# Performance work log

Hardware: AMD Instinct MI355X
Metric: run time of the kernel (lower is better)

The kernel has to match this reference:

```python
import jax, jax.numpy as jnp
import numpy as np

D = 1024      # model dim (used for theta exponent and 1/sqrt(d) scale)
D_H = 128     # head dim


def make_theta():
    # theta[i] = 10 ** (-2*(i-1)/d), each value repeated twice -> length d_H
    i = np.repeat(np.arange(D_H // 2), 2)
    return jnp.asarray(10.0 ** (-2.0 * (i - 1) / D), dtype=jnp.float32)


def rotation(x, theta):
    # x: [B, T, d_H]; positions are 1..T (source uses arange(1, T+1))
    B, T, dh = x.shape
    idx = jnp.arange(1, T + 1, dtype=x.dtype)[:, None]          # [T, 1]
    ang = idx * theta[None, :]                                   # [T, d_H]
    cos, sin = jnp.cos(ang), jnp.sin(ang)
    # pairwise swap with sign: (x0, x1) -> (x1, -x0)
    x2 = x.reshape(B, T, dh // 2, 2)
    swapped = jnp.stack([x2[..., 1], -x2[..., 0]], axis=-1).reshape(B, T, dh)
    return x * cos + swapped * sin


def setup_inputs() -> dict:
    key = jax.random.key(0)
    kx, kq, kk, kv = jax.random.split(key, 4)
    B, T = 4, 2048
    scale = 1.0 / np.sqrt(D)
    return {
        "x": jax.random.normal(kx, (B, T, D), dtype=jnp.float32),
        "Wq": jax.random.normal(kq, (D_H, D), dtype=jnp.float32) * scale,
        "Wk": jax.random.normal(kk, (D_H, D), dtype=jnp.float32) * scale,
        "Wv": jax.random.normal(kv, (D_H, D), dtype=jnp.float32) * scale,
        "theta": make_theta(),
    }


def reference(x, Wq, Wk, Wv, theta):
    B, T, d = x.shape
    Q = jnp.einsum('btd,hd->bth', x, Wq)
    K = jnp.einsum('btd,hd->bth', x, Wk)
    V = jnp.einsum('btd,hd->bth', x, Wv)
    Q = rotation(Q, theta)
    K = rotation(K, theta)
    # scale uses model dim d (not d_H), as in the source
    scores = jnp.einsum('bqh,bkh->bqk', Q, K) * (d ** -0.5)
    causal = jnp.tril(jnp.ones((T, T), dtype=bool))
    scores = jnp.where(causal, scores, -jnp.inf)
    attn = jax.nn.softmax(scores, axis=-1)
    return jnp.einsum('bqk,bkh->bqh', attn, V)
```

## Files before the change

kernel.cpp:

```cpp
#include <hip/hip_runtime.h>
#include <math.h>

#define T_SEQ 2048
#define D_MODEL 1024
#define DH 128
#define SLOTS 288
#define FRAG_B 262144

typedef __bf16 bfx8 __attribute__((ext_vector_type(8)));
typedef float f32x4 __attribute__((ext_vector_type(4)));

union U16x8 { uint4 u4; unsigned int ui[4]; unsigned short us[8]; __bf16 bf[8]; bfx8 v; };

__device__ inline uint4 cvt8u(float4 a, float4 b) {
    U16x8 u;
    u.bf[0] = (__bf16)a.x; u.bf[1] = (__bf16)a.y; u.bf[2] = (__bf16)a.z; u.bf[3] = (__bf16)a.w;
    u.bf[4] = (__bf16)b.x; u.bf[5] = (__bf16)b.y; u.bf[6] = (__bf16)b.z; u.bf[7] = (__bf16)b.w;
    return u.u4;
}

__device__ inline int slot_base32(int qt) {
    int g = qt >> 3, j = qt & 7;
    return 4 * g * (g + 1) + j * (g + 1);
}

__global__ __launch_bounds__(256) void wcvt_kernel(
    const float* __restrict__ Wq, const float* __restrict__ Wk,
    const float* __restrict__ Wv, __bf16* __restrict__ Wb)
{
    const int i = blockIdx.x * 256 + threadIdx.x;
    const int plane = i >> 14;
    const int off = (i & 16383) * 8;
    const float* src = (plane == 0) ? Wq : (plane == 1) ? Wk : Wv;
    float4 a = *(const float4*)(src + off);
    float4 b = *(const float4*)(src + off + 4);
    *(uint4*)&Wb[(size_t)plane * (DH * D_MODEL) + off] = cvt8u(a, b);
}

__global__ __launch_bounds__(256) void qkv_kernel(
    const float* __restrict__ x, const __bf16* __restrict__ Wb,
    const float* __restrict__ theta,
    __bf16* __restrict__ QF, __bf16* __restrict__ KF, __bf16* __restrict__ VF, int M)
{
    __shared__ __align__(16) unsigned short As[2][64 * 72];
    __shared__ __align__(16) unsigned short Bs[2][128 * 72];

    const int ntile = M / 64;
    const int bx = blockIdx.x;
    const int wsel = bx / ntile;
    const int m0 = (bx - wsel * ntile) * 64;

    const int tid = threadIdx.x;
    const int ln = tid & 63, wv = tid >> 6;
    const int lo = ln & 15, quad = ln >> 4;
    const int hi8 = quad * 8;
    const int wm = (wv & 1) * 32;
    const int wn = (wv >> 1) * 64;

    const int arow = tid >> 2, aseg = (tid & 3) * 16;
    const int brow = tid >> 1, bseg = (tid & 1) * 32;
    const float*  axp = x + (size_t)(m0 + arow) * D_MODEL + aseg;
    const __bf16* bwp = Wb + (size_t)wsel * (DH * D_MODEL) + (size_t)brow * D_MODEL + bseg;

    float4 ar[4];
    uint4  br[4];
    #pragma unroll
    for (int q = 0; q < 4; ++q) ar[q] = *(const float4*)(axp + q * 4);
    #pragma unroll
    for (int q = 0; q < 4; ++q) br[q] = *(const uint4*)(bwp + q * 8);

    *(uint4*)&As[0][arow * 72 + aseg]     = cvt8u(ar[0], ar[1]);
    *(uint4*)&As[0][arow * 72 + aseg + 8] = cvt8u(ar[2], ar[3]);
    #pragma unroll
    for (int q = 0; q < 4; ++q) *(uint4*)&Bs[0][brow * 72 + bseg + q * 8] = br[q];
    __syncthreads();

    f32x4 acc[2][4];
    #pragma unroll
    for (int i = 0; i < 2; ++i)
        #pragma unroll
        for (int j = 0; j < 4; ++j) acc[i][j] = (f32x4)(0.f);

    for (int s = 0; s < 16; ++s) {
        const int cur = s & 1;
        if (s < 15) {
            const int kc = (s + 1) * 64;
            #pragma unroll
            for (int q = 0; q < 4; ++q) ar[q] = *(const float4*)(axp + kc + q * 4);
            #pragma unroll
            for (int q = 0; q < 4; ++q) br[q] = *(const uint4*)(bwp + kc + q * 8);
        }

        bfx8 af[2][2], bfr[4][2];
        #pragma unroll
        for (int i = 0; i < 2; ++i)
            #pragma unroll
            for (int s2 = 0; s2 < 2; ++s2)
                af[i][s2] = *(const bfx8*)&As[cur][(wm + i * 16 + lo) * 72 + s2 * 32 + hi8];
        #pragma unroll
        for (int j = 0; j < 4; ++j)
            #pragma unroll
            for (int s2 = 0; s2 < 2; ++s2)
                bfr[j][s2] = *(const bfx8*)&Bs[cur][(wn + j * 16 + lo) * 72 + s2 * 32 + hi8];
        #pragma unroll
        for (int s2 = 0; s2 < 2; ++s2)
            #pragma unroll
            for (int i = 0; i < 2; ++i)
                #pragma unroll
                for (int j = 0; j < 4; ++j)
                    acc[i][j] = __builtin_amdgcn_mfma_f32_16x16x32_bf16(af[i][s2], bfr[j][s2], acc[i][j], 0, 0, 0);

        if (s < 15) {
            const int nxt = cur ^ 1;
            *(uint4*)&As[nxt][arow * 72 + aseg]     = cvt8u(ar[0], ar[1]);
            *(uint4*)&As[nxt][arow * 72 + aseg + 8] = cvt8u(ar[2], ar[3]);
            #pragma unroll
            for (int q = 0; q < 4; ++q) *(uint4*)&Bs[nxt][brow * 72 + bseg + q * 8] = br[q];
            __syncthreads();
        }
    }

    const int b = m0 >> 11;
    const int mloc0 = m0 & (T_SEQ - 1);

    if (wsel < 2) {
        __syncthreads();
        unsigned short* T = &Bs[0][0];
        #pragma unroll
        for (int j = 0; j < 4; ++j) {
            const int h = wn + j * 16 + lo;
            const float th = theta[h];
            #pragma unroll
            for (int i = 0; i < 2; ++i) {
                #pragma unroll
                for (int r = 0; r < 4; ++r) {
                    const int mloc = wm + i * 16 + quad * 4 + r;
                    float v = acc[i][j][r];
                    float partner = __shfl_xor(v, 1, 64);
                    float ang = (float)(mloc0 + mloc + 1) * th;
                    float rev = ang * 0.15915494309189535f;
                    rev -= floorf(rev);
                    float sn = __builtin_amdgcn_sinf(rev);
                    float cs = __builtin_amdgcn_cosf(rev);
                    float res = (h & 1) ? (v * cs - partner * sn)
                                        : (v * cs + partner * sn);
                    U16x8 u; u.bf[0] = (__bf16)res;
                    T[mloc * 136 + h] = u.us[0];
                }
            }
        }
        __syncthreads();
        const int g = tid >> 6, L = tid & 63;
        const int lo2 = L & 15, q2 = L >> 4;
        __bf16* dst = (wsel == 0 ? QF : KF) + (size_t)b * FRAG_B
                    + (size_t)(((mloc0 >> 4) + g) * 4) * 512 + L * 8;
        #pragma unroll
        for (int c4 = 0; c4 < 4; ++c4)
            *(uint4*)(dst + c4 * 512) = *(const uint4*)&T[(g * 16 + lo2) * 136 + c4 * 32 + q2 * 8];
    } else {
        __syncthreads();
        unsigned short* VT = &As[0][0];
        #pragma unroll
        for (int j = 0; j < 4; ++j) {
            const int h = wn + j * 16 + lo;
            #pragma unroll
            for (int i = 0; i < 2; ++i)
                #pragma unroll
                for (int r = 0; r < 4; ++r) {
                    U16x8 u; u.bf[0] = (__bf16)acc[i][j][r];
                    VT[h * 72 + wm + i * 16 + quad * 4 + r] = u.us[0];
                }
        }
        __syncthreads();
        const int g = tid >> 6, L = tid & 63;
        const int lo2 = L & 15, q2 = L >> 4;
        const int kb = mloc0 >> 5;
        #pragma unroll
        for (int f = 0; f < 4; ++f) {
            const int fid = g * 4 + f;
            const int kt = fid >> 3, j = fid & 7;
            __bf16* dst = VF + (size_t)b * FRAG_B + (size_t)((kb + kt) * 8 + j) * 512 + L * 8;
            *(uint4*)dst = *(const uint4*)&VT[(j * 16 + lo2) * 72 + kt * 32 + q2 * 8];
        }
    }
}

__global__ __launch_bounds__(64) void attn_partial_kernel(
    const __bf16* __restrict__ QF, const __bf16* __restrict__ KF,
    const __bf16* __restrict__ VF,
    __bf16* __restrict__ Opb, float* __restrict__ Ll)
{
    const int qt = blockIdx.x, c = blockIdx.y, b = blockIdx.z;
    const int qbase = qt * 32;
    const int kstart = c << 8;
    if (kstart > qbase) return;
    const int nt = min(8, (qbase + 32 - kstart) >> 5);

    __shared__ __align__(16) unsigned short Pw[2 * 640];

    const int ln = threadIdx.x;
    const int lo = ln & 15, quad = ln >> 4;
    const int hi8 = quad * 8;

    const __bf16* QFb = QF + (size_t)b * FRAG_B;
    const __bf16* KFb = KF + (size_t)b * FRAG_B;
    const __bf16* VFb = VF + (size_t)b * FRAG_B;

    bfx8 qf[2][4];
    #pragma unroll
    for (int iq = 0; iq < 2; ++iq)
        #pragma unroll
        for (int c4 = 0; c4 < 4; ++c4)
            qf[iq][c4] = *(const bfx8*)&QFb[(size_t)((qt * 2 + iq) * 4 + c4) * 512 + ln * 8];

    f32x4 O[2][8];
    #pragma unroll
    for (int iq = 0; iq < 2; ++iq)
        #pragma unroll
        for (int j = 0; j < 8; ++j) O[iq][j] = (f32x4)(0.f);
    float lsum[2][4];
    #pragma unroll
    for (int iq = 0; iq < 2; ++iq)
        #pragma unroll
        for (int r = 0; r < 4; ++r) lsum[iq][r] = 0.f;

    for (int kt = 0; kt < nt; ++kt) {
        const int k0 = kstart + kt * 32;
        const int kt16 = k0 >> 4;
        bfx8 kf[2][4], vf[8];
        #pragma unroll
        for (int jj = 0; jj < 2; ++jj)
            #pragma unroll
            for (int c4 = 0; c4 < 4; ++c4)
                kf[jj][c4] = *(const bfx8*)&KFb[(size_t)((kt16 + jj) * 4 + c4) * 512 + ln * 8];
        #pragma unroll
        for (int j = 0; j < 8; ++j)
            vf[j] = *(const bfx8*)&VFb[(size_t)((k0 >> 5) * 8 + j) * 512 + ln * 8];

        f32x4 s4[2][2];
        #pragma unroll
        for (int iq = 0; iq < 2; ++iq)
            #pragma unroll
            for (int jj = 0; jj < 2; ++jj) s4[iq][jj] = (f32x4)(0.f);
        #pragma unroll
        for (int c4 = 0; c4 < 4; ++c4)
            #pragma unroll
            for (int iq = 0; iq < 2; ++iq)
                #pragma unroll
                for (int jj = 0; jj < 2; ++jj)
                    s4[iq][jj] = __builtin_amdgcn_mfma_f32_16x16x32_bf16(qf[iq][c4], kf[jj][c4], s4[iq][jj], 0, 0, 0);

        const bool needMask = (k0 + 31 > qbase);
        #pragma unroll
        for (int iq = 0; iq < 2; ++iq)
            #pragma unroll
            for (int jj = 0; jj < 2; ++jj)
                #pragma unroll
                for (int r = 0; r < 4; ++r) {
                    const int col = k0 + jj * 16 + lo;
                    const int row = qbase + iq * 16 + quad * 4 + r;
                    float p = __expf(s4[iq][jj][r] * 0.03125f);
                    if (needMask && col > row) p = 0.f;
                    lsum[iq][r] += p;
                    U16x8 u; u.bf[0] = (__bf16)p;
                    Pw[iq * 640 + (quad * 4 + r) * 40 + jj * 16 + lo] = u.us[0];
                }

        bfx8 pf0 = *(const bfx8*)&Pw[lo * 40 + hi8];
        bfx8 pf1 = *(const bfx8*)&Pw[640 + lo * 40 + hi8];
        #pragma unroll
        for (int j = 0; j < 8; ++j) {
            O[0][j] = __builtin_amdgcn_mfma_f32_16x16x32_bf16(pf0, vf[j], O[0][j], 0, 0, 0);
            O[1][j] = __builtin_amdgcn_mfma_f32_16x16x32_bf16(pf1, vf[j], O[1][j], 0, 0, 0);
        }
    }

    #pragma unroll
    for (int off = 1; off < 16; off <<= 1)
        #pragma unroll
        for (int iq = 0; iq < 2; ++iq)
            #pragma unroll
            for (int r = 0; r < 4; ++r) lsum[iq][r] += __shfl_xor(lsum[iq][r], off, 64);

    const size_t sb = (size_t)b * SLOTS + slot_base32(qt) + c;
    #pragma unroll
    for (int iq = 0; iq < 2; ++iq)
        #pragma unroll
        for (int j = 0; j < 8; ++j) {
            U16x8 u;
            u.bf[0] = (__bf16)O[iq][j][0]; u.bf[1] = (__bf16)O[iq][j][1];
            u.bf[2] = (__bf16)O[iq][j][2]; u.bf[3] = (__bf16)O[iq][j][3];
            *(uint2*)&Opb[((sb * 2 + iq) * 8 + j) * 256 + ln * 4] = make_uint2(u.ui[0], u.ui[1]);
        }
    if (lo == 0) {
        #pragma unroll
        for (int iq = 0; iq < 2; ++iq)
            #pragma unroll
            for (int r = 0; r < 4; ++r)
                Ll[sb * 32 + iq * 16 + quad * 4 + r] = lsum[iq][r];
    }
}

__global__ __launch_bounds__(128) void attn_merge_kernel(
    const __bf16* __restrict__ Opb, const float* __restrict__ Ll,
    float* __restrict__ out)
{
    const int qt = blockIdx.x, b = blockIdx.y, j = blockIdx.z;
    const int g = qt >> 3, nc = g + 1;
    const size_t base = (size_t)b * SLOTS + slot_base32(qt);

    __shared__ float Lsh[8][32];
    const int tid = threadIdx.x;
    const int iq = tid >> 6, ln = tid & 63;
    const int lo = ln & 15, quad = ln >> 4;

    for (int idx = tid; idx < nc * 32; idx += 128)
        Lsh[idx >> 5][idx & 31] = Ll[(base + (idx >> 5)) * 32 + (idx & 31)];
    __syncthreads();

    float acc[4] = {0.f, 0.f, 0.f, 0.f};
    for (int cc = 0; cc < nc; ++cc) {
        uint2 d = *(const uint2*)&Opb[(((base + cc) * 2 + iq) * 8 + j) * 256 + ln * 4];
        U16x8 u; u.ui[0] = d.x; u.ui[1] = d.y;
        #pragma unroll
        for (int r = 0; r < 4; ++r) acc[r] += (float)u.bf[r];
    }

    #pragma unroll
    for (int r = 0; r < 4; ++r) {
        const int row = iq * 16 + quad * 4 + r;
        float l = 0.f;
        for (int cc = 0; cc < nc; ++cc) l += Lsh[cc][row];
        out[((size_t)b * T_SEQ + qt * 32 + row) * DH + j * 16 + lo] = acc[r] / l;
    }
}

extern "C" void kernel_launch(void* const* d_in, const int* in_sizes, int n_in,
                              void* d_out, int out_size, void* d_ws, size_t ws_size,
                              hipStream_t stream) {
    const float* x     = (const float*)d_in[0];
    const float* Wq    = (const float*)d_in[1];
    const float* Wk    = (const float*)d_in[2];
    const float* Wv    = (const float*)d_in[3];
    const float* theta = (const float*)d_in[4];
    float* out = (float*)d_out;

    const int M = in_sizes[0] / D_MODEL;
    const int B = M / T_SEQ;

    __bf16* QF  = (__bf16*)d_ws;
    __bf16* KF  = QF + (size_t)B * FRAG_B;
    __bf16* VF  = KF + (size_t)B * FRAG_B;
    __bf16* Opb = VF + (size_t)B * FRAG_B;
    float*  Ll  = (float*)(Opb + (size_t)B * SLOTS * 2 * 8 * 256);
    __bf16* Wb  = Opb;

    wcvt_kernel<<<dim3(192), 256, 0, stream>>>(Wq, Wk, Wv, Wb);
    qkv_kernel<<<dim3(3 * (M / 64)), 256, 0, stream>>>(x, Wb, theta, QF, KF, VF, M);
    attn_partial_kernel<<<dim3(T_SEQ / 32, 8, B), 64, 0, stream>>>(QF, KF, VF, Opb, Ll);
    attn_merge_kernel<<<dim3(T_SEQ / 32, B, 8), 128, 0, stream>>>(Opb, Ll, out);
}
```

Before: 126.6 us.

## Replace split-K partial buffers and merge with atomic fp32 accumulation; prefetch K fragments

Partial attention outputs are no longer written as bf16 slots and reduced by a separate merge kernel. Each block now atomically adds its fp32 O and row sums into a zeroed accumulator, and a simple normalize kernel divides by the sum. This drops the slot indexing and the bf16 rounding of partials, but adds a zeroing kernel and many scalar global atomics. K fragments for the next tile are also loaded one iteration ahead to hide load latency.

```diff
diff --git a/kernel.cpp b/kernel.cpp
--- a/kernel.cpp
+++ b/kernel.cpp
@@ -4,7 +4,6 @@
 #define T_SEQ 2048
 #define D_MODEL 1024
 #define DH 128
-#define SLOTS 288
 #define FRAG_B 262144
 
 typedef __bf16 bfx8 __attribute__((ext_vector_type(8)));
@@ -17,11 +16,6 @@
     u.bf[0] = (__bf16)a.x; u.bf[1] = (__bf16)a.y; u.bf[2] = (__bf16)a.z; u.bf[3] = (__bf16)a.w;
     u.bf[4] = (__bf16)b.x; u.bf[5] = (__bf16)b.y; u.bf[6] = (__bf16)b.z; u.bf[7] = (__bf16)b.w;
     return u.u4;
-}
-
-__device__ inline int slot_base32(int qt) {
-    int g = qt >> 3, j = qt & 7;
-    return 4 * g * (g + 1) + j * (g + 1);
 }
 
 __global__ __launch_bounds__(256) void wcvt_kernel(
@@ -35,6 +29,12 @@
     float4 a = *(const float4*)(src + off);
     float4 b = *(const float4*)(src + off + 4);
     *(uint4*)&Wb[(size_t)plane * (DH * D_MODEL) + off] = cvt8u(a, b);
+}
+
+__global__ __launch_bounds__(256) void zero_kernel(float* __restrict__ p)
+{
+    const size_t i = ((size_t)blockIdx.x * 256 + threadIdx.x) * 4;
+    *(float4*)(p + i) = make_float4(0.f, 0.f, 0.f, 0.f);
 }
 
 __global__ __launch_bounds__(256) void qkv_kernel(
@@ -188,7 +188,7 @@
 __global__ __launch_bounds__(64) void attn_partial_kernel(
     const __bf16* __restrict__ QF, const __bf16* __restrict__ KF,
     const __bf16* __restrict__ VF,
-    __bf16* __restrict__ Opb, float* __restrict__ Ll)
+    float* __restrict__ Oacc, float* __restrict__ Lacc)
 {
     const int qt = blockIdx.x, c = blockIdx.y, b = blockIdx.z;
     const int qbase = qt * 32;
@@ -224,18 +224,27 @@
         #pragma unroll
         for (int r = 0; r < 4; ++r) lsum[iq][r] = 0.f;
 
+    bfx8 kcur[2][4], knxt[2][4];
+    #pragma unroll
+    for (int jj = 0; jj < 2; ++jj)
+        #pragma unroll
+        for (int c4 = 0; c4 < 4; ++c4)
+            kcur[jj][c4] = *(const bfx8*)&KFb[(size_t)(((kstart >> 4) + jj) * 4 + c4) * 512 + ln * 8];
+
     for (int kt = 0; kt < nt; ++kt) {
         const int k0 = kstart + kt * 32;
-        const int kt16 = k0 >> 4;
-        bfx8 kf[2][4], vf[8];
-        #pragma unroll
-        for (int jj = 0; jj < 2; ++jj)
-            #pragma unroll
-            for (int c4 = 0; c4 < 4; ++c4)
-                kf[jj][c4] = *(const bfx8*)&KFb[(size_t)((kt16 + jj) * 4 + c4) * 512 + ln * 8];
+        bfx8 vf[8];
         #pragma unroll
         for (int j = 0; j < 8; ++j)
             vf[j] = *(const bfx8*)&VFb[(size_t)((k0 >> 5) * 8 + j) * 512 + ln * 8];
+        if (kt + 1 < nt) {
+            const int kn16 = (k0 + 32) >> 4;
+            #pragma unroll
+            for (int jj = 0; jj < 2; ++jj)
+                #pragma unroll
+                for (int c4 = 0; c4 < 4; ++c4)
+                    knxt[jj][c4] = *(const bfx8*)&KFb[(size_t)((kn16 + jj) * 4 + c4) * 512 + ln * 8];
+        }
 
         f32x4 s4[2][2];
         #pragma unroll
@@ -248,7 +257,7 @@
             for (int iq = 0; iq < 2; ++iq)
                 #pragma unroll
                 for (int jj = 0; jj < 2; ++jj)
-                    s4[iq][jj] = __builtin_amdgcn_mfma_f32_16x16x32_bf16(qf[iq][c4], kf[jj][c4], s4[iq][jj], 0, 0, 0);
+                    s4[iq][jj] = __builtin_amdgcn_mfma_f32_16x16x32_bf16(qf[iq][c4], kcur[jj][c4], s4[iq][jj], 0, 0, 0);
 
         const bool needMask = (k0 + 31 > qbase);
         #pragma unroll
@@ -273,6 +282,11 @@
             O[0][j] = __builtin_amdgcn_mfma_f32_16x16x32_bf16(pf0, vf[j], O[0][j], 0, 0, 0);
             O[1][j] = __builtin_amdgcn_mfma_f32_16x16x32_bf16(pf1, vf[j], O[1][j], 0, 0, 0);
         }
+
+        #pragma unroll
+        for (int jj = 0; jj < 2; ++jj)
+            #pragma unroll
+            for (int c4 = 0; c4 < 4; ++c4) kcur[jj][c4] = knxt[jj][c4];
     }
 
     #pragma unroll
@@ -282,57 +296,40 @@
             #pragma unroll
             for (int r = 0; r < 4; ++r) lsum[iq][r] += __shfl_xor(lsum[iq][r], off, 64);
 
-    const size_t sb = (size_t)b * SLOTS + slot_base32(qt) + c;
+    float* Ob = Oacc + (size_t)b * T_SEQ * DH;
     #pragma unroll
     for (int iq = 0; iq < 2; ++iq)
         #pragma unroll
         for (int j = 0; j < 8; ++j) {
-            U16x8 u;
-            u.bf[0] = (__bf16)O[iq][j][0]; u.bf[1] = (__bf16)O[iq][j][1];
-            u.bf[2] = (__bf16)O[iq][j][2]; u.bf[3] = (__bf16)O[iq][j][3];
-            *(uint2*)&Opb[((sb * 2 + iq) * 8 + j) * 256 + ln * 4] = make_uint2(u.ui[0], u.ui[1]);
+            const int col = j * 16 + lo;
+            #pragma unroll
+            for (int r = 0; r < 4; ++r) {
+                const int row = qbase + iq * 16 + quad * 4 + r;
+                unsafeAtomicAdd(&Ob[(size_t)row * DH + col], O[iq][j][r]);
+            }
         }
     if (lo == 0) {
         #pragma unroll
         for (int iq = 0; iq < 2; ++iq)
             #pragma unroll
             for (int r = 0; r < 4; ++r)
-                Ll[sb * 32 + iq * 16 + quad * 4 + r] = lsum[iq][r];
+                unsafeAtomicAdd(&Lacc[(size_t)b * T_SEQ + qbase + iq * 16 + quad * 4 + r],
+                                lsum[iq][r]);
     }
 }
 
-__global__ __launch_bounds__(128) void attn_merge_kernel(
-    const __bf16* __restrict__ Opb, const float* __restrict__ Ll,
+__global__ __launch_bounds__(256) void normalize_kernel(
+    const float* __restrict__ Oacc, const float* __restrict__ Lacc,
     float* __restrict__ out)
 {
-    const int qt = blockIdx.x, b = blockIdx.y, j = blockIdx.z;
-    const int g = qt >> 3, nc = g + 1;
-    const size_t base = (size_t)b * SLOTS + slot_base32(qt);
-
-    __shared__ float Lsh[8][32];
-    const int tid = threadIdx.x;
-    const int iq = tid >> 6, ln = tid & 63;
-    const int lo = ln & 15, quad = ln >> 4;
-
-    for (int idx = tid; idx < nc * 32; idx += 128)
-        Lsh[idx >> 5][idx & 31] = Ll[(base + (idx >> 5)) * 32 + (idx & 31)];
-    __syncthreads();
-
-    float acc[4] = {0.f, 0.f, 0.f, 0.f};
-    for (int cc = 0; cc < nc; ++cc) {
-        uint2 d = *(const uint2*)&Opb[(((base + cc) * 2 + iq) * 8 + j) * 256 + ln * 4];
-        U16x8 u; u.ui[0] = d.x; u.ui[1] = d.y;
-        #pragma unroll
-        for (int r = 0; r < 4; ++r) acc[r] += (float)u.bf[r];
-    }
-
-    #pragma unroll
-    for (int r = 0; r < 4; ++r) {
-        const int row = iq * 16 + quad * 4 + r;
-        float l = 0.f;
-        for (int cc = 0; cc < nc; ++cc) l += Lsh[cc][row];
-        out[((size_t)b * T_SEQ + qt * 32 + row) * DH + j * 16 + lo] = acc[r] / l;
-    }
+    const int gid = blockIdx.x * 256 + threadIdx.x;
+    const int row = gid >> 4;
+    const int d0  = (gid & 15) * 8;
+    const float inv = 1.f / Lacc[row];
+    float4 a = *(const float4*)(Oacc + (size_t)row * DH + d0);
+    float4 b = *(const float4*)(Oacc + (size_t)row * DH + d0 + 4);
+    *(float4*)(out + (size_t)row * DH + d0)     = make_float4(a.x*inv, a.y*inv, a.z*inv, a.w*inv);
+    *(float4*)(out + (size_t)row * DH + d0 + 4) = make_float4(b.x*inv, b.y*inv, b.z*inv, b.w*inv);
 }
 
 extern "C" void kernel_launch(void* const* d_in, const int* in_sizes, int n_in,
@@ -348,15 +345,16 @@
     const int M = in_sizes[0] / D_MODEL;
     const int B = M / T_SEQ;
 
-    __bf16* QF  = (__bf16*)d_ws;
-    __bf16* KF  = QF + (size_t)B * FRAG_B;
-    __bf16* VF  = KF + (size_t)B * FRAG_B;
-    __bf16* Opb = VF + (size_t)B * FRAG_B;
-    float*  Ll  = (float*)(Opb + (size_t)B * SLOTS * 2 * 8 * 256);
-    __bf16* Wb  = Opb;
+    __bf16* QF   = (__bf16*)d_ws;
+    __bf16* KF   = QF + (size_t)B * FRAG_B;
+    __bf16* VF   = KF + (size_t)B * FRAG_B;
+    float*  Oacc = (float*)(VF + (size_t)B * FRAG_B);
+    float*  Lacc = Oacc + (size_t)B * T_SEQ * DH;
+    __bf16* Wb   = (__bf16*)Oacc;
 
     wcvt_kernel<<<dim3(192), 256, 0, stream>>>(Wq, Wk, Wv, Wb);
     qkv_kernel<<<dim3(3 * (M / 64)), 256, 0, stream>>>(x, Wb, theta, QF, KF, VF, M);
-    attn_partial_kernel<<<dim3(T_SEQ / 32, 8, B), 64, 0, stream>>>(QF, KF, VF, Opb, Ll);
-    attn_merge_kernel<<<dim3(T_SEQ / 32, B, 8), 128, 0, stream>>>(Opb, Ll, out);
-}
+    zero_kernel<<<dim3((B * T_SEQ * DH + B * T_SEQ) / 1024), 256, 0, stream>>>(Oacc);
+    attn_partial_kernel<<<dim3(T_SEQ / 32, 8, B), 64, 0, stream>>>(QF, KF, VF, Oacc, Lacc);
+    normalize_kernel<<<dim3(B * T_SEQ * DH / 2048), 256, 0, stream>>>(Oacc, Lacc, out);
+}
```

After: 133.4 us. +5.4%, slower.

## Pre-convert x and weights to MFMA fragment layout; single-wave QKV GEMM; prefetch K

Applied to the files above, without the earlier changes.

A new prep kernel converts x and the three weight matrices to bf16 and stores them directly in MFMA fragment order. The QKV projection then becomes a 64-thread kernel that streams fragments from global memory with register double buffering and uses no shared-memory staging or block barriers. The attention kernel now prefetches the next K tile into registers while the current one is being processed. The cost is an extra full pass that writes and re-reads x in bf16, plus higher register pressure and a grid of more, smaller blocks.

```diff
diff --git a/kernel.cpp b/kernel.cpp
--- a/kernel.cpp
+++ b/kernel.cpp
@@ -24,99 +24,100 @@
     return 4 * g * (g + 1) + j * (g + 1);
 }
 
-__global__ __launch_bounds__(256) void wcvt_kernel(
+__global__ __launch_bounds__(256) void prep_kernel(
+    const float* __restrict__ x,
     const float* __restrict__ Wq, const float* __restrict__ Wk,
-    const float* __restrict__ Wv, __bf16* __restrict__ Wb)
+    const float* __restrict__ Wv,
+    __bf16* __restrict__ xF, __bf16* __restrict__ WF, int nxb)
 {
-    const int i = blockIdx.x * 256 + threadIdx.x;
-    const int plane = i >> 14;
-    const int off = (i & 16383) * 8;
-    const float* src = (plane == 0) ? Wq : (plane == 1) ? Wk : Wv;
-    float4 a = *(const float4*)(src + off);
-    float4 b = *(const float4*)(src + off + 4);
-    *(uint4*)&Wb[(size_t)plane * (DH * D_MODEL) + off] = cvt8u(a, b);
-}
-
-__global__ __launch_bounds__(256) void qkv_kernel(
-    const float* __restrict__ x, const __bf16* __restrict__ Wb,
+    const int bi = blockIdx.x;
+    const int tid = threadIdx.x;
+
+    if (bi < nxb) {
+        __shared__ __align__(16) unsigned short Xs[64 * 72];
+        const int m0 = (bi >> 4) * 64;
+        const int k0 = (bi & 15) * 64;
+        const int row = tid >> 2, cs = (tid & 3) * 16;
+        const float* xp = x + (size_t)(m0 + row) * D_MODEL + k0 + cs;
+        float4 a0 = *(const float4*)xp;
+        float4 a1 = *(const float4*)(xp + 4);
+        float4 a2 = *(const float4*)(xp + 8);
+        float4 a3 = *(const float4*)(xp + 12);
+        *(uint4*)&Xs[row * 72 + cs]     = cvt8u(a0, a1);
+        *(uint4*)&Xs[row * 72 + cs + 8] = cvt8u(a2, a3);
+        __syncthreads();
+        const int L = tid & 63;
+        #pragma unroll
+        for (int rr = 0; rr < 2; ++rr) {
+            const int fid = rr * 4 + (tid >> 6);
+            const int mtl = fid >> 1, kcl = fid & 1;
+            uint4 d = *(const uint4*)&Xs[(mtl * 16 + (L & 15)) * 72 + kcl * 32 + (L >> 4) * 8];
+            const size_t frag = (size_t)((m0 >> 4) + mtl) * 32 + (k0 >> 5) + kcl;
+            *(uint4*)&xF[frag * 512 + L * 8] = d;
+        }
+    } else {
+        const int i = (bi - nxb) * 256 + tid;
+        const int wsel = i >> 14;
+        const int i2 = i & 16383;
+        const int kc = i2 >> 9, j = (i2 >> 6) & 7, ln = i2 & 63;
+        const int lo = ln & 15, quad = ln >> 4;
+        const float* src = (wsel == 0) ? Wq : (wsel == 1) ? Wk : Wv;
+        const float* p = src + (size_t)(j * 16 + lo) * D_MODEL + kc * 32 + quad * 8;
+        float4 a = *(const float4*)p;
+        float4 b = *(const float4*)(p + 4);
+        *(uint4*)&WF[(size_t)((wsel * 32 + kc) * 8 + j) * 512 + ln * 8] = cvt8u(a, b);
+    }
+}
+
+__global__ __launch_bounds__(64) void qkv_kernel(
+    const __bf16* __restrict__ xF, const __bf16* __restrict__ WF,
     const float* __restrict__ theta,
-    __bf16* __restrict__ QF, __bf16* __restrict__ KF, __bf16* __restrict__ VF, int M)
+    __bf16* __restrict__ QF, __bf16* __restrict__ KF, __bf16* __restrict__ VF)
 {
-    __shared__ __align__(16) unsigned short As[2][64 * 72];
-    __shared__ __align__(16) unsigned short Bs[2][128 * 72];
-
-    const int ntile = M / 64;
+    __shared__ __align__(16) unsigned short T[32 * 136];
+
     const int bx = blockIdx.x;
-    const int wsel = bx / ntile;
-    const int m0 = (bx - wsel * ntile) * 64;
-
-    const int tid = threadIdx.x;
-    const int ln = tid & 63, wv = tid >> 6;
+    const int wsel = bx >> 8;
+    const int m0 = (bx & 255) * 32;
+
+    const int ln = threadIdx.x;
     const int lo = ln & 15, quad = ln >> 4;
-    const int hi8 = quad * 8;
-    const int wm = (wv & 1) * 32;
-    const int wn = (wv >> 1) * 64;
-
-    const int arow = tid >> 2, aseg = (tid & 3) * 16;
-    const int brow = tid >> 1, bseg = (tid & 1) * 32;
-    const float*  axp = x + (size_t)(m0 + arow) * D_MODEL + aseg;
-    const __bf16* bwp = Wb + (size_t)wsel * (DH * D_MODEL) + (size_t)brow * D_MODEL + bseg;
-
-    float4 ar[4];
-    uint4  br[4];
-    #pragma unroll
-    for (int q = 0; q < 4; ++q) ar[q] = *(const float4*)(axp + q * 4);
-    #pragma unroll
-    for (int q = 0; q < 4; ++q) br[q] = *(const uint4*)(bwp + q * 8);
-
-    *(uint4*)&As[0][arow * 72 + aseg]     = cvt8u(ar[0], ar[1]);
-    *(uint4*)&As[0][arow * 72 + aseg + 8] = cvt8u(ar[2], ar[3]);
-    #pragma unroll
-    for (int q = 0; q < 4; ++q) *(uint4*)&Bs[0][brow * 72 + bseg + q * 8] = br[q];
-    __syncthreads();
-
-    f32x4 acc[2][4];
-    #pragma unroll
-    for (int i = 0; i < 2; ++i)
-        #pragma unroll
-        for (int j = 0; j < 4; ++j) acc[i][j] = (f32x4)(0.f);
-
-    for (int s = 0; s < 16; ++s) {
-        const int cur = s & 1;
-        if (s < 15) {
-            const int kc = (s + 1) * 64;
-            #pragma unroll
-            for (int q = 0; q < 4; ++q) ar[q] = *(const float4*)(axp + kc + q * 4);
-            #pragma unroll
-            for (int q = 0; q < 4; ++q) br[q] = *(const uint4*)(bwp + kc + q * 8);
-        }
-
-        bfx8 af[2][2], bfr[4][2];
-        #pragma unroll
-        for (int i = 0; i < 2; ++i)
-            #pragma unroll
-            for (int s2 = 0; s2 < 2; ++s2)
-                af[i][s2] = *(const bfx8*)&As[cur][(wm + i * 16 + lo) * 72 + s2 * 32 + hi8];
-        #pragma unroll
-        for (int j = 0; j < 4; ++j)
-            #pragma unroll
-            for (int s2 = 0; s2 < 2; ++s2)
-                bfr[j][s2] = *(const bfx8*)&Bs[cur][(wn + j * 16 + lo) * 72 + s2 * 32 + hi8];
-        #pragma unroll
-        for (int s2 = 0; s2 < 2; ++s2)
-            #pragma unroll
-            for (int i = 0; i < 2; ++i)
-                #pragma unroll
-                for (int j = 0; j < 4; ++j)
-                    acc[i][j] = __builtin_amdgcn_mfma_f32_16x16x32_bf16(af[i][s2], bfr[j][s2], acc[i][j], 0, 0, 0);
-
-        if (s < 15) {
-            const int nxt = cur ^ 1;
-            *(uint4*)&As[nxt][arow * 72 + aseg]     = cvt8u(ar[0], ar[1]);
-            *(uint4*)&As[nxt][arow * 72 + aseg + 8] = cvt8u(ar[2], ar[3]);
-            #pragma unroll
-            for (int q = 0; q < 4; ++q) *(uint4*)&Bs[nxt][brow * 72 + bseg + q * 8] = br[q];
-            __syncthreads();
+
+    const __bf16* WFp = WF + (size_t)wsel * (32 * 8 * 512);
+    const size_t xf0 = ((size_t)(m0 >> 4)) * 32;
+
+    bfx8 xc[2], xn[2], wc[8], wn[8];
+    #pragma unroll
+    for (int iq = 0; iq < 2; ++iq)
+        xc[iq] = *(const bfx8*)&xF[(xf0 + iq * 32) * 512 + ln * 8];
+    #pragma unroll
+    for (int j = 0; j < 8; ++j)
+        wc[j] = *(const bfx8*)&WFp[(size_t)j * 512 + ln * 8];
+
+    f32x4 acc[2][8];
+    #pragma unroll
+    for (int iq = 0; iq < 2; ++iq)
+        #pragma unroll
+        for (int j = 0; j < 8; ++j) acc[iq][j] = (f32x4)(0.f);
+
+    for (int kc = 0; kc < 32; ++kc) {
+        if (kc < 31) {
+            #pragma unroll
+            for (int iq = 0; iq < 2; ++iq)
+                xn[iq] = *(const bfx8*)&xF[(xf0 + iq * 32 + kc + 1) * 512 + ln * 8];
+            #pragma unroll
+            for (int j = 0; j < 8; ++j)
+                wn[j] = *(const bfx8*)&WFp[(size_t)((kc + 1) * 8 + j) * 512 + ln * 8];
+        }
+        #pragma unroll
+        for (int j = 0; j < 8; ++j) {
+            acc[0][j] = __builtin_amdgcn_mfma_f32_16x16x32_bf16(xc[0], wc[j], acc[0][j], 0, 0, 0);
+            acc[1][j] = __builtin_amdgcn_mfma_f32_16x16x32_bf16(xc[1], wc[j], acc[1][j], 0, 0, 0);
+        }
+        if (kc < 31) {
+            xc[0] = xn[0]; xc[1] = xn[1];
+            #pragma unroll
+            for (int j = 0; j < 8; ++j) wc[j] = wn[j];
         }
     }
 
@@ -124,20 +125,20 @@
     const int mloc0 = m0 & (T_SEQ - 1);
 
     if (wsel < 2) {
-        __syncthreads();
-        unsigned short* T = &Bs[0][0];
-        #pragma unroll
-        for (int j = 0; j < 4; ++j) {
-            const int h = wn + j * 16 + lo;
-            const float th = theta[h];
-            #pragma unroll
-            for (int i = 0; i < 2; ++i) {
+        __bf16* dstP = (wsel == 0 ? QF : KF) + (size_t)b * FRAG_B;
+        const int t16l = mloc0 >> 4;
+        #pragma unroll
+        for (int iq = 0; iq < 2; ++iq) {
+            #pragma unroll
+            for (int j = 0; j < 8; ++j) {
+                const int h = j * 16 + lo;
+                const float th = theta[h];
                 #pragma unroll
                 for (int r = 0; r < 4; ++r) {
-                    const int mloc = wm + i * 16 + quad * 4 + r;
-                    float v = acc[i][j][r];
+                    const int pos = mloc0 + iq * 16 + quad * 4 + r + 1;
+                    float v = acc[iq][j][r];
                     float partner = __shfl_xor(v, 1, 64);
-                    float ang = (float)(mloc0 + mloc + 1) * th;
+                    float ang = (float)pos * th;
                     float rev = ang * 0.15915494309189535f;
                     rev -= floorf(rev);
                     float sn = __builtin_amdgcn_sinf(rev);
@@ -145,42 +146,34 @@
                     float res = (h & 1) ? (v * cs - partner * sn)
                                         : (v * cs + partner * sn);
                     U16x8 u; u.bf[0] = (__bf16)res;
-                    T[mloc * 136 + h] = u.us[0];
+                    T[(quad * 4 + r) * 136 + h] = u.us[0];
                 }
             }
-        }
-        __syncthreads();
-        const int g = tid >> 6, L = tid & 63;
-        const int lo2 = L & 15, q2 = L >> 4;
-        __bf16* dst = (wsel == 0 ? QF : KF) + (size_t)b * FRAG_B
-                    + (size_t)(((mloc0 >> 4) + g) * 4) * 512 + L * 8;
-        #pragma unroll
-        for (int c4 = 0; c4 < 4; ++c4)
-            *(uint4*)(dst + c4 * 512) = *(const uint4*)&T[(g * 16 + lo2) * 136 + c4 * 32 + q2 * 8];
+            #pragma unroll
+            for (int c4 = 0; c4 < 4; ++c4) {
+                uint4 d = *(const uint4*)&T[(ln & 15) * 136 + c4 * 32 + (ln >> 4) * 8];
+                *(uint4*)&dstP[(size_t)((t16l + iq) * 4 + c4) * 512 + ln * 8] = d;
+            }
+        }
     } else {
-        __syncthreads();
-        unsigned short* VT = &As[0][0];
-        #pragma unroll
-        for (int j = 0; j < 4; ++j) {
-            const int h = wn + j * 16 + lo;
-            #pragma unroll
-            for (int i = 0; i < 2; ++i)
+        const int kt32 = mloc0 >> 5;
+        #pragma unroll
+        for (int iq = 0; iq < 2; ++iq)
+            #pragma unroll
+            for (int j = 0; j < 8; ++j)
                 #pragma unroll
                 for (int r = 0; r < 4; ++r) {
-                    U16x8 u; u.bf[0] = (__bf16)acc[i][j][r];
-                    VT[h * 72 + wm + i * 16 + quad * 4 + r] = u.us[0];
+                    U16x8 u; u.bf[0] = (__bf16)acc[iq][j][r];
+                    T[(iq * 16 + quad * 4 + r) * 136 + j * 16 + lo] = u.us[0];
                 }
-        }
-        __syncthreads();
-        const int g = tid >> 6, L = tid & 63;
-        const int lo2 = L & 15, q2 = L >> 4;
-        const int kb = mloc0 >> 5;
-        #pragma unroll
-        for (int f = 0; f < 4; ++f) {
-            const int fid = g * 4 + f;
-            const int kt = fid >> 3, j = fid & 7;
-            __bf16* dst = VF + (size_t)b * FRAG_B + (size_t)((kb + kt) * 8 + j) * 512 + L * 8;
-            *(uint4*)dst = *(const uint4*)&VT[(j * 16 + lo2) * 72 + kt * 32 + q2 * 8];
+        __bf16* dstP = VF + (size_t)b * FRAG_B;
+        #pragma unroll
+        for (int j = 0; j < 8; ++j) {
+            U16x8 u;
+            #pragma unroll
+            for (int e = 0; e < 8; ++e)
+                u.us[e] = T[((ln >> 4) * 8 + e) * 136 + j * 16 + (ln & 15)];
+            *(uint4*)&dstP[(size_t)(kt32 * 8 + j) * 512 + ln * 8] = u.u4;
         }
     }
 }
@@ -224,18 +217,27 @@
         #pragma unroll
         for (int r = 0; r < 4; ++r) lsum[iq][r] = 0.f;
 
+    bfx8 kcur[2][4], knxt[2][4];
+    #pragma unroll
+    for (int jj = 0; jj < 2; ++jj)
+        #pragma unroll
+        for (int c4 = 0; c4 < 4; ++c4)
+            kcur[jj][c4] = *(const bfx8*)&KFb[(size_t)(((kstart >> 4) + jj) * 4 + c4) * 512 + ln * 8];
+
     for (int kt = 0; kt < nt; ++kt) {
         const int k0 = kstart + kt * 32;
-        const int kt16 = k0 >> 4;
-        bfx8 kf[2][4], vf[8];
-        #pragma unroll
-        for (int jj = 0; jj < 2; ++jj)
-            #pragma unroll
-            for (int c4 = 0; c4 < 4; ++c4)
-                kf[jj][c4] = *(const bfx8*)&KFb[(size_t)((kt16 + jj) * 4 + c4) * 512 + ln * 8];
+        bfx8 vf[8];
         #pragma unroll
         for (int j = 0; j < 8; ++j)
             vf[j] = *(const bfx8*)&VFb[(size_t)((k0 >> 5) * 8 + j) * 512 + ln * 8];
+        if (kt + 1 < nt) {
+            const int kn16 = (k0 + 32) >> 4;
+            #pragma unroll
+            for (int jj = 0; jj < 2; ++jj)
+                #pragma unroll
+                for (int c4 = 0; c4 < 4; ++c4)
+                    knxt[jj][c4] = *(const bfx8*)&KFb[(size_t)((kn16 + jj) * 4 + c4) * 512 + ln * 8];
+        }
 
         f32x4 s4[2][2];
         #pragma unroll
@@ -248,7 +250,7 @@
             for (int iq = 0; iq < 2; ++iq)
                 #pragma unroll
                 for (int jj = 0; jj < 2; ++jj)
-                    s4[iq][jj] = __builtin_amdgcn_mfma_f32_16x16x32_bf16(qf[iq][c4], kf[jj][c4], s4[iq][jj], 0, 0, 0);
+                    s4[iq][jj] = __builtin_amdgcn_mfma_f32_16x16x32_bf16(qf[iq][c4], kcur[jj][c4], s4[iq][jj], 0, 0, 0);
 
         const bool needMask = (k0 + 31 > qbase);
         #pragma unroll
@@ -273,6 +275,11 @@
             O[0][j] = __builtin_amdgcn_mfma_f32_16x16x32_bf16(pf0, vf[j], O[0][j], 0, 0, 0);
             O[1][j] = __builtin_amdgcn_mfma_f32_16x16x32_bf16(pf1, vf[j], O[1][j], 0, 0, 0);
         }
+
+        #pragma unroll
+        for (int jj = 0; jj < 2; ++jj)
+            #pragma unroll
+            for (int c4 = 0; c4 < 4; ++c4) kcur[jj][c4] = knxt[jj][c4];
     }
 
     #pragma unroll
@@ -348,15 +355,17 @@
     const int M = in_sizes[0] / D_MODEL;
     const int B = M / T_SEQ;
 
-    __bf16* QF  = (__bf16*)d_ws;
+    __bf16* xF  = (__bf16*)d_ws;
+    __bf16* WF  = xF + (size_t)M * D_MODEL;
+    __bf16* QF  = WF + (size_t)3 * 32 * 8 * 512;
     __bf16* KF  = QF + (size_t)B * FRAG_B;
     __bf16* VF  = KF + (size_t)B * FRAG_B;
     __bf16* Opb = VF + (size_t)B * FRAG_B;
     float*  Ll  = (float*)(Opb + (size_t)B * SLOTS * 2 * 8 * 256);
-    __bf16* Wb  = Opb;
-
-    wcvt_kernel<<<dim3(192), 256, 0, stream>>>(Wq, Wk, Wv, Wb);
-    qkv_kernel<<<dim3(3 * (M / 64)), 256, 0, stream>>>(x, Wb, theta, QF, KF, VF, M);
+
+    const int nxb = (M / 64) * 16;
+    prep_kernel<<<dim3(nxb + 192), 256, 0, stream>>>(x, Wq, Wk, Wv, xF, WF, nxb);
+    qkv_kernel<<<dim3(3 * (M / 32)), 64, 0, stream>>>(xF, WF, theta, QF, KF, VF);
     attn_partial_kernel<<<dim3(T_SEQ / 32, 8, B), 64, 0, stream>>>(QF, KF, VF, Opb, Ll);
     attn_merge_kernel<<<dim3(T_SEQ / 32, B, 8), 128, 0, stream>>>(Opb, Ll, out);
 }
```

New measurement: 124.6 us. Within noise of the previous version (-1.6%).
